# Performance work log

Hardware: AMD Instinct MI355X
Metric: run time of the kernel (lower is better)

The kernel has to match this reference:

```python
import jax, jax.numpy as jnp
import numpy as np

ALPHA = 0.1
MAX_ITER = 35
TOL = 0.01
STEP = ALPHA / 2.0  # step_size = alpha/2 as in TV2DFunction.forward


def _prox_tv1d(step, y):
    """Exact 1D TV prox via taut-string lower/upper hulls (faithful port of _prox_tv1d)."""
    n = y.shape[0]
    width = n + 1
    dt = y.dtype
    cs = jnp.cumsum(y)
    y_low = jnp.concatenate([jnp.zeros(1, dt), cs - step]).at[width - 1].add(step)
    y_up = jnp.concatenate([jnp.zeros(1, dt), cs + step]).at[width - 1].add(-step)

    inf = jnp.asarray(jnp.inf, dt)
    il = jnp.zeros(width, jnp.int32)   # index_low
    iu = jnp.zeros(width, jnp.int32)   # index_up
    idx = jnp.zeros(width, jnp.int32)  # breakpoint indices
    sl = jnp.zeros(width, dt).at[0].set(inf)    # slope_low
    su = jnp.zeros(width, dt).at[0].set(-inf)   # slope_up
    z = jnp.zeros(width, dt)
    zero = jnp.int32(0)

    def fdiv(num, a, b):
        # a > b always holds on the taken branch; maximum() only guards the
        # unselected jnp.where branch against NaN/Inf.
        return num / jnp.maximum(a - b, 1).astype(dt)

    def body(i, st):
        il, sl, iu, su, idx, z, s_l, c_l, s_u, c_u, c = st
        c_l = c_l + 1
        c_u = c_u + 1
        il = il.at[c_l].set(i)
        iu = iu.at[c_u].set(i)
        sl = sl.at[c_l].set(y_low[i] - y_low[i - 1])

        def w1_cond(t):
            il_, sl_, c_l_ = t
            return (c_l_ > s_l + 1) & (sl_[jnp.maximum(s_l, c_l_ - 1)] <= sl_[c_l_])

        def w1_body(t):
            il_, sl_, c_l_ = t
            c_l_ = c_l_ - 1
            il_ = il_.at[c_l_].set(i)
            ns = jnp.where(c_l_ > s_l + 1,
                           fdiv(y_low[i] - y_low[il_[c_l_ - 1]], i, il_[c_l_ - 1]),
                           fdiv(y_low[i] - z[c], i, idx[c]))
            return il_, sl_.at[c_l_].set(ns), c_l_

        il, sl, c_l = jax.lax.while_loop(w1_cond, w1_body, (il, sl, c_l))

        su = su.at[c_u].set(y_up[i] - y_up[i - 1])

        def w2_cond(t):
            iu_, su_, c_u_ = t
            return (c_u_ > s_u + 1) & (su_[jnp.maximum(s_u, c_u_ - 1)] >= su_[c_u_])

        def w2_body(t):
            iu_, su_, c_u_ = t
            c_u_ = c_u_ - 1
            iu_ = iu_.at[c_u_].set(i)
            ns = jnp.where(c_u_ > s_u + 1,
                           fdiv(y_up[i] - y_up[iu_[c_u_ - 1]], i, iu_[c_u_ - 1]),
                           fdiv(y_up[i] - z[c], i, idx[c]))
            return iu_, su_.at[c_u_].set(ns), c_u_

        iu, su, c_u = jax.lax.while_loop(w2_cond, w2_body, (iu, su, c_u))

        def w3_cond(t):
            idx_, z_, sl_, il_, s_u_, c_ = t
            return (c_l == s_l + 1) & (c_u > s_u_ + 1) & (sl_[c_l] >= su[s_u_ + 1])

        def w3_body(t):
            idx_, z_, sl_, il_, s_u_, c_ = t
            c_ = c_ + 1
            s_u_ = s_u_ + 1
            k = iu[s_u_]
            idx_ = idx_.at[c_].set(k)
            z_ = z_.at[c_].set(y_up[k])
            il_ = il_.at[s_l].set(k)
            sl_ = sl_.at[c_l].set(fdiv(y_low[i] - y_up[k], i, k))
            return idx_, z_, sl_, il_, s_u_, c_

        idx, z, sl, il, s_u, c = jax.lax.while_loop(w3_cond, w3_body, (idx, z, sl, il, s_u, c))

        def w4_cond(t):
            idx_, z_, su_, iu_, s_l_, c_ = t
            return (c_u == s_u + 1) & (c_l > s_l_ + 1) & (su_[c_u] <= sl[s_l_ + 1])

        def w4_body(t):
            idx_, z_, su_, iu_, s_l_, c_ = t
            c_ = c_ + 1
            s_l_ = s_l_ + 1
            k = il[s_l_]
            idx_ = idx_.at[c_].set(k)
            z_ = z_.at[c_].set(y_low[k])
            iu_ = iu_.at[s_u].set(k)
            su_ = su_.at[c_u].set(fdiv(y_up[i] - y_low[k], i, k))
            return idx_, z_, su_, iu_, s_l_, c_

        idx, z, su, iu, s_l, c = jax.lax.while_loop(w4_cond, w4_body, (idx, z, su, iu, s_l, c))

        return il, sl, iu, su, idx, z, s_l, c_l, s_u, c_u, c

    st = (il, sl, iu, su, idx, z, zero, zero, zero, zero, zero)
    il, sl, iu, su, idx, z, s_l, c_l, s_u, c_u, c = jax.lax.fori_loop(1, width, body, st)

    # tail: append remaining lower-hull points to the breakpoint list
    m = c_l - s_l
    offs = jnp.arange(width)
    valid = (offs >= 1) & (offs <= m)
    src = il[jnp.clip(s_l + offs, 0, width - 1)]
    tgt = jnp.where(valid, c + offs, width)  # 'width' is out of bounds -> dropped
    idx = idx.at[tgt].set(src, mode='drop')
    z = z.at[tgt].set(y_low[src], mode='drop')
    c = c + m

    # piecewise-constant output: slope of taut string on each segment
    a = (z - jnp.roll(z, 1)) / jnp.maximum(idx - jnp.roll(idx, 1), 1).astype(dt)
    knots = jnp.where(offs <= c, idx, n + 1)  # sorted; idx[c] == n
    seg = jnp.searchsorted(knots, jnp.arange(n), side='right')  # segment id in [1, c]
    return a[seg]


def _prox_cols(step, A):
    return jax.vmap(lambda col: _prox_tv1d(step, col), in_axes=1, out_axes=1)(A)


def _prox_rows(step, A):
    return jax.vmap(lambda row: _prox_tv1d(step, row))(A)


def _prox_tv2d(x, step, max_iter, tol):
    """Douglas-Rachford splitting for 2D TV prox (Barbero & Sra 2014)."""
    def cond(carry):
        it, x_, p, q, acc = carry
        return (it < max_iter) & (acc >= tol)

    def body(carry):
        it, x_, p, q, _ = carry
        y = _prox_cols(step, x_ + p)
        p = p + x_ - y
        x2 = _prox_rows(step, y + q)
        q = q + y - x2
        acc = jnp.max(jnp.abs(y - x2))
        return it + 1, x2, p, q, acc

    z0 = jnp.zeros_like(x)
    init = (jnp.int32(0), x, z0, z0, jnp.asarray(jnp.inf, x.dtype))
    return jax.lax.while_loop(cond, body, init)[1]


def setup_inputs() -> dict:
    key = jax.random.key(0)
    X = jax.random.normal(key, (256, 256), dtype=jnp.float32)
    return {"X": X}


def reference(X):
    return _prox_tv2d(X, STEP, MAX_ITER, TOL)
```

## Files before the change

kernel.cpp:

```cpp
#include <hip/hip_runtime.h>

#define N 256
#define NLINE 4
#define NB (N / NLINE)
#define NT (NLINE * 64)
#define LAM 0.05f
#define TWOLAM (2.0f * LAM)
#define FOURLAM (4.0f * LAM)
#define MAXIT 35
#define TOL 0.01f
#define SLOTSTRIDE 4

__device__ __forceinline__ float rlane(float v, int lane) {
    return __int_as_float(__builtin_amdgcn_readlane(__float_as_int(v), lane));
}

__device__ __forceinline__ void gstore(float* p, float v) {
    __hip_atomic_store(p, v, __ATOMIC_RELAXED, __HIP_MEMORY_SCOPE_AGENT);
}
__device__ __forceinline__ float4 gload4(const float* p) {
    float4 r;
    asm volatile("global_load_dwordx4 %0, %1, off sc0 sc1\n\ts_waitcnt vmcnt(0)"
                 : "=&v"(r) : "v"(p) : "memory");
    return r;
}

struct Dist { float r0, r1, r2, r3; };

__device__ __forceinline__ float dfetch(const Dist& d, int k) {
    const int lane = k & 63;
    const int sel = k >> 6;
    float a = rlane(d.r0, lane);
    float b = rlane(d.r1, lane);
    float c = rlane(d.r2, lane);
    float e = rlane(d.r3, lane);
    float ab = (sel & 1) ? b : a;
    float ce = (sel & 1) ? e : c;
    return (sel & 2) ? ce : ab;
}

__device__ __forceinline__ void flushseg(Dist& o, int lo, int hi, float val, int lane) {
    const unsigned len = (unsigned)(hi - lo);
    const int base = lane - lo;
    o.r0 = ((unsigned)(base      ) <= len) ? val : o.r0;
    o.r1 = ((unsigned)(base + 64 ) <= len) ? val : o.r1;
    o.r2 = ((unsigned)(base + 128) <= len) ? val : o.r2;
    o.r3 = ((unsigned)(base + 192) <= len) ? val : o.r3;
}

__device__ __forceinline__ unsigned long long sel4(unsigned long long a, unsigned long long b,
                                                   unsigned long long c, unsigned long long d, int r) {
    unsigned long long ab = (r & 1) ? b : a;
    unsigned long long cd = (r & 1) ? d : c;
    return (r & 2) ? cd : ab;
}

__device__ __forceinline__ unsigned wredmax(unsigned x) {
    unsigned t;
    t = (unsigned)__builtin_amdgcn_update_dpp(0, (int)x, 0x111, 0xf, 0xf, true); x = x > t ? x : t;
    t = (unsigned)__builtin_amdgcn_update_dpp(0, (int)x, 0x112, 0xf, 0xf, true); x = x > t ? x : t;
    t = (unsigned)__builtin_amdgcn_update_dpp(0, (int)x, 0x114, 0xf, 0xf, true); x = x > t ? x : t;
    t = (unsigned)__builtin_amdgcn_update_dpp(0, (int)x, 0x118, 0xf, 0xf, true); x = x > t ? x : t;
    t = (unsigned)__builtin_amdgcn_update_dpp(0, (int)x, 0x142, 0xf, 0xf, true); x = x > t ? x : t;
    t = (unsigned)__builtin_amdgcn_update_dpp(0, (int)x, 0x143, 0xf, 0xf, true); x = x > t ? x : t;
    return (unsigned)__builtin_amdgcn_readlane((int)x, 63);
}

__device__ void tv1d_scan(const Dist& v, Dist& o, const int lane)
{
    const float lam = LAM, mlam = -LAM, twolam = TWOLAM;

    Dist vnx;
    {
        float a0 = __shfl_down(v.r0, 1), a1 = __shfl_down(v.r1, 1);
        float a2 = __shfl_down(v.r2, 1), a3 = __shfl_down(v.r3, 1);
        const bool hi = (lane == 63);
        vnx.r0 = hi ? rlane(v.r1, 0) : a0;
        vnx.r1 = hi ? rlane(v.r2, 0) : a1;
        vnx.r2 = hi ? rlane(v.r3, 0) : a2;
        vnx.r3 = hi ? v.r3 : a3;
    }
    Dist d;
    d.r0 = vnx.r0 - v.r0;  d.r1 = vnx.r1 - v.r1;
    d.r2 = vnx.r2 - v.r2;  d.r3 = vnx.r3 - v.r3;
    const unsigned lambits = __float_as_uint(lam);
    Dist sl;
    sl.r0 = __uint_as_float((__float_as_uint(d.r0) & 0x80000000u) | lambits);
    sl.r1 = __uint_as_float((__float_as_uint(d.r1) & 0x80000000u) | lambits);
    sl.r2 = __uint_as_float((__float_as_uint(d.r2) & 0x80000000u) | lambits);
    sl.r3 = __uint_as_float((__float_as_uint(d.r3) & 0x80000000u) | lambits);
    Dist slp;
    {
        float b0 = __shfl_up(sl.r0, 1), b1 = __shfl_up(sl.r1, 1);
        float b2 = __shfl_up(sl.r2, 1), b3 = __shfl_up(sl.r3, 1);
        const bool lo = (lane == 0);
        slp.r0 = lo ? 0.0f : b0;
        slp.r1 = lo ? rlane(sl.r0, 63) : b1;
        slp.r2 = lo ? rlane(sl.r1, 63) : b2;
        slp.r3 = lo ? rlane(sl.r2, 63) : b3;
    }
    Dist e, g;
    {
        float t0 = v.r0 - slp.r0, t1 = v.r1 - slp.r1, t2 = v.r2 - slp.r2, t3 = v.r3 - slp.r3;
        e.r0 = t0 + sl.r0;  e.r1 = t1 + sl.r1;  e.r2 = t2 + sl.r2;  e.r3 = t3 + sl.r3;
        g.r0 = t0 - lam;    g.r1 = t1 - lam;    g.r2 = t2 - lam;    g.r3 = t3 - lam;
    }
    const unsigned long long S0 = __ballot(d.r0 < 0.0f);
    const unsigned long long S1 = __ballot(d.r1 < 0.0f);
    const unsigned long long S2 = __ballot(d.r2 < 0.0f);
    const unsigned long long S3 = __ballot(d.r3 < 0.0f);
    const unsigned long long B20 = __ballot(fabsf(d.r0) > TWOLAM);
    const unsigned long long B21 = __ballot(fabsf(d.r1) > TWOLAM);
    const unsigned long long B22 = __ballot(fabsf(d.r2) > TWOLAM);
    const unsigned long long B23 = __ballot(fabsf(d.r3) > TWOLAM);
    const unsigned long long B40 = __ballot(fabsf(d.r0) > FOURLAM);
    const unsigned long long B41 = __ballot(fabsf(d.r1) > FOURLAM);
    const unsigned long long B42 = __ballot(fabsf(d.r2) > FOURLAM);
    const unsigned long long B43 = __ballot(fabsf(d.r3) > FOURLAM);
    const unsigned long long Sp0 = (S0 << 1);
    const unsigned long long Sp1 = (S1 << 1) | (S0 >> 63);
    const unsigned long long Sp2 = (S2 << 1) | (S1 >> 63);
    const unsigned long long Sp3 = (S3 << 1) | (S2 >> 63);
    const unsigned long long NF0 = ~(B40 | (B20 & ~(S0 ^ Sp0)));
    const unsigned long long NF1 = ~(B41 | (B21 & ~(S1 ^ Sp1)));
    const unsigned long long NF2 = ~(B42 | (B22 & ~(S2 ^ Sp2)));
    const unsigned long long NF3 = ~((B43 | (B23 & ~(S3 ^ Sp3))) & 0x7FFFFFFFFFFFFFFFull);
    const unsigned long long FNn0 = (S0 & B20) | (~S0 & B40);
    const unsigned long long FNn1 = (S1 & B21) | (~S1 & B41);
    const unsigned long long FNn2 = (S2 & B22) | (~S2 & B42);
    const unsigned long long FNn3 = (S3 & B23) | (~S3 & B43);
    const unsigned long long FNp0 = (~S0 & B20) | (S0 & B40);
    const unsigned long long FNp1 = (~S1 & B21) | (S1 & B41);
    const unsigned long long FNp2 = (~S2 & B22) | (S2 & B42);
    const unsigned long long FNp3 = (~S3 & B23) | (S3 & B43);
    const int initFF = (int)(B40 & 1ull);

    auto firstnf = [&](int jmin) -> int {
        const int w = jmin >> 6;
        unsigned long long m = sel4(NF0, NF1, NF2, NF3, w) >> (jmin & 63);
        if (m) return jmin + (int)__builtin_ctzll(m);
        unsigned long long m1 = (w < 1) ? NF1 : 0ull;
        unsigned long long m2 = (w < 2) ? NF2 : 0ull;
        if (m1) return 64 + (int)__builtin_ctzll(m1);
        if (m2) return 128 + (int)__builtin_ctzll(m2);
        return 192 + (int)__builtin_ctzll(NF3);
    };

    auto trigbit = [&](int kk, int neg) -> int {
        const int w = kk >> 6;
        const unsigned long long m = neg ? sel4(FNn0, FNn1, FNn2, FNn3, w)
                                         : sel4(FNp0, FNp1, FNp2, FNp3, w);
        return (int)((m >> (kk & 63)) & 1ull);
    };

    int k = 0, k0 = 0, km = 0, kp = 0;
    float umin = lam, umax = mlam;
    const float v0 = rlane(v.r0, 0);
    float vmin = v0 - lam, vmax = v0 + lam;
    float flen = 1.0f;
    float rnext = 0.5f;
    float vn1 = rlane(vnx.r0, 0);

    auto fastfwd = [&]() {
        const int K1 = firstnf(k + 1);
        const int sneg = (int)((sel4(S0, S1, S2, S3, k >> 6) >> (k & 63)) & 1ull);
        flushseg(o, k, k, sneg ? vmin : vmax, lane);
        if (K1 > k + 1) {
            const int lo = k + 1;
            const unsigned len = (unsigned)(K1 - 1 - lo);
            const int base = lane - lo;
            o.r0 = ((unsigned)(base      ) <= len) ? e.r0 : o.r0;
            o.r1 = ((unsigned)(base + 64 ) <= len) ? e.r1 : o.r1;
            o.r2 = ((unsigned)(base + 128) <= len) ? e.r2 : o.r2;
            o.r3 = ((unsigned)(base + 192) <= len) ? e.r3 : o.r3;
        }
        k = K1; k0 = K1; km = K1; kp = K1;
        vmin = dfetch(g, K1);
        vmax = vmin + twolam;
        umin = lam; umax = mlam;
        flen = 1.0f; rnext = 0.5f;
        vn1 = dfetch(vnx, K1);
    };

    auto do_step = [&]() {
        const float pf_nj = dfetch(vnx, k + 1);
        const float pf_n  = dfetch(vnx, km + 1);
        const float pf_p  = dfetch(vnx, kp + 1);
        const float un = umin + vn1 - vmin;
        const float ux = umax + vn1 - vmax;
        const bool neg = un < mlam;
        const bool pos = ux > lam;
        const int wn = (k + 1) >> 6, bn = (k + 1) & 63;
        const int tn = (int)((sel4(FNn0, FNn1, FNn2, FNn3, wn) >> bn) & 1ull);
        const int tp = (int)((sel4(FNp0, FNp1, FNp2, FNp3, wn) >> bn) & 1ull);
        if (__builtin_expect((int)(neg | pos), 1)) {
            const float fval = neg ? vmin : vmax;
            const int   fhi  = neg ? km : kp;
            flushseg(o, k0, fhi, fval, lane);
            const int k0n = fhi + 1;
            float vstar;
            int trig;
            if (__builtin_expect((int)(k0n <= k), 0)) {
                vstar = dfetch(v, k0n);
                trig = trigbit(k0n, (int)neg);
            } else {
                vstar = vn1;
                trig = neg ? tn : tp;
            }
            k = k0n; k0 = k0n; km = k0n; kp = k0n;
            vmin = neg ? vstar : vstar - twolam;
            vmax = vmin + twolam;
            umin = lam; umax = mlam;
            flen = 1.0f; rnext = 0.5f;
            if (k < N - 1 && trig) {
                fastfwd();
            } else {
                vn1 = neg ? pf_n : pf_p;
            }
        } else {
            k++;
            const float r = rnext;
            flen += 1.0f;
            const bool cmin = (un >= lam);
            const bool cmax = (ux <= mlam);
            vmin = cmin ? fmaf(un - lam, r, vmin) : vmin;
            km   = cmin ? k : km;
            umin = cmin ? lam : un;
            vmax = cmax ? fmaf(ux + lam, r, vmax) : vmax;
            kp   = cmax ? k : kp;
            umax = cmax ? mlam : ux;
            vn1 = pf_nj;
            rnext = __builtin_amdgcn_rcpf(flen + 1.0f);
        }
    };

    if (initFF) fastfwd();

    for (;;) {
        while (k < N - 1) {
            do_step();
            if (k >= N - 1) break;
            do_step();
        }
        for (;;) {
            if (umin < 0.0f) {
                flushseg(o, k0, km, vmin, lane);
                k0 = km + 1;
                if (k0 > N - 1) return;
                km = k = k0;
                vmin = dfetch(v, k0);
                umin = lam;
                umax = vmin + lam - vmax;
                flen = 1.0f;
            } else if (umax > 0.0f) {
                flushseg(o, k0, kp, vmax, lane);
                k0 = kp + 1;
                if (k0 > N - 1) return;
                kp = k = k0;
                vmax = dfetch(v, k0);
                umax = mlam;
                umin = vmax - lam - vmin;
                flen = 1.0f;
            } else {
                vmin += umin / flen;
                flushseg(o, k0, k, vmin, lane);
                return;
            }
            if (k != N - 1) break;
        }
        rnext = 0.5f;
        vn1 = dfetch(vnx, k);
    }
}

template <bool WANT>
__device__ __forceinline__ unsigned wavebar(unsigned long long* slots, unsigned seq,
                                            unsigned payload, int line, int lane, int wave,
                                            unsigned long long* s_rel)
{
    __builtin_amdgcn_s_waitcnt(0);
    __hip_atomic_store(&slots[line * SLOTSTRIDE],
                       ((unsigned long long)payload << 32) | (unsigned long long)seq,
                       __ATOMIC_RELAXED, __HIP_MEMORY_SCOPE_AGENT);
    unsigned ga = 0u;
    if (wave == 0) {
        auto ld = [&](int i) {
            return __hip_atomic_load(&slots[i * SLOTSTRIDE],
                                     __ATOMIC_RELAXED, __HIP_MEMORY_SCOPE_AGENT);
        };
        unsigned long long f0 = ld(lane), f1 = ld(lane + 64),
                           f2 = ld(lane + 128), f3 = ld(lane + 192);
        for (;;) {
            unsigned long long g0 = ld(lane), g1 = ld(lane + 64),
                               g2 = ld(lane + 128), g3 = ld(lane + 192);
            const bool ok = ((unsigned)f0 >= seq) & ((unsigned)f1 >= seq) &
                            ((unsigned)f2 >= seq) & ((unsigned)f3 >= seq);
            if (__all((int)ok)) break;
            f0 = g0; f1 = g1; f2 = g2; f3 = g3;
        }
        if (WANT) {
            unsigned a = (unsigned)(f0 >> 32), b = (unsigned)(f1 >> 32);
            unsigned c = (unsigned)(f2 >> 32), d = (unsigned)(f3 >> 32);
            a = a > b ? a : b;  c = c > d ? c : d;  a = a > c ? a : c;
            ga = wredmax(a);
        }
        if (lane == 0)
            __hip_atomic_store(s_rel, ((unsigned long long)ga << 32) | (unsigned long long)seq,
                               __ATOMIC_RELAXED, __HIP_MEMORY_SCOPE_WORKGROUP);
    } else {
        unsigned long long r;
        do {
            r = __hip_atomic_load(s_rel, __ATOMIC_RELAXED, __HIP_MEMORY_SCOPE_WORKGROUP);
        } while ((unsigned)r < seq);
        if (WANT) ga = (unsigned)(r >> 32);
    }
    return ga;
}

__global__ __launch_bounds__(NT) void tv2d_coop(const float* __restrict__ X,
                                                float* __restrict__ xw,
                                                float* __restrict__ y,
                                                unsigned long long* __restrict__ slots)
{
    const int t = threadIdx.x;
    const int lane = t & 63;
    const int wave = t >> 6;
    const int line = blockIdx.x * NLINE + wave;
    const int col4 = 4 * blockIdx.x;
    __shared__ float tile[N * 5];
    __shared__ unsigned long long s_rel;
    if (t == 0) s_rel = 0ull;

    Dist p = {0.f, 0.f, 0.f, 0.f};
    Dist q = {0.f, 0.f, 0.f, 0.f};
    unsigned accprev = 0u;

    for (int it = 0; it < MAXIT; ++it) {
        const float* xs = (it == 0) ? X : xw;
        const float4 xc = gload4(xs + t * N + col4);
        tile[t * 5 + 0] = xc.x;
        tile[t * 5 + 1] = xc.y;
        tile[t * 5 + 2] = xc.z;
        tile[t * 5 + 3] = xc.w;
        __syncthreads();
        Dist v, o;
        v.r0 = tile[(lane      ) * 5 + wave] + p.r0;
        v.r1 = tile[(lane + 64 ) * 5 + wave] + p.r1;
        v.r2 = tile[(lane + 128) * 5 + wave] + p.r2;
        v.r3 = tile[(lane + 192) * 5 + wave] + p.r3;
        tv1d_scan(v, o, lane);
        p.r0 = v.r0 - o.r0;  p.r1 = v.r1 - o.r1;
        p.r2 = v.r2 - o.r2;  p.r3 = v.r3 - o.r3;
        float* yt = y + line * N;
        gstore(yt + lane,       o.r0);
        gstore(yt + lane + 64,  o.r1);
        gstore(yt + lane + 128, o.r2);
        gstore(yt + lane + 192, o.r3);
        wavebar<false>(slots, 2u * (unsigned)it + 1u, accprev, line, lane, wave, &s_rel);

        const float4 yc = gload4(y + t * N + col4);
        tile[t * 5 + 0] = yc.x;
        tile[t * 5 + 1] = yc.y;
        tile[t * 5 + 2] = yc.z;
        tile[t * 5 + 3] = yc.w;
        __syncthreads();
        float y0 = tile[(lane      ) * 5 + wave];
        float y1 = tile[(lane + 64 ) * 5 + wave];
        float y2 = tile[(lane + 128) * 5 + wave];
        float y3 = tile[(lane + 192) * 5 + wave];
        Dist w, o2;
        w.r0 = y0 + q.r0;
        w.r1 = y1 + q.r1;
        w.r2 = y2 + q.r2;
        w.r3 = y3 + q.r3;
        tv1d_scan(w, o2, lane);
        float d0 = y0 - o2.r0;
        float d1 = y1 - o2.r1;
        float d2 = y2 - o2.r2;
        float d3 = y3 - o2.r3;
        q.r0 = w.r0 - o2.r0;  q.r1 = w.r1 - o2.r1;
        q.r2 = w.r2 - o2.r2;  q.r3 = w.r3 - o2.r3;
        float* xr = xw + line * N;
        gstore(xr + lane,       o2.r0);
        gstore(xr + lane + 64,  o2.r1);
        gstore(xr + lane + 128, o2.r2);
        gstore(xr + lane + 192, o2.r3);

        float am = fmaxf(fmaxf(fabsf(d0), fabsf(d1)), fmaxf(fabsf(d2), fabsf(d3)));
        const unsigned acc = wredmax(__float_as_uint(am));

        if (it == MAXIT - 1) break;

        const unsigned ga = wavebar<true>(slots, 2u * (unsigned)it + 2u, acc, line, lane, wave, &s_rel);
        if (__uint_as_float(ga) < TOL) break;
        accprev = acc;
    }
}

extern "C" void kernel_launch(void* const* d_in, const int* in_sizes, int n_in,
                              void* d_out, int out_size, void* d_ws, size_t ws_size,
                              hipStream_t stream) {
    const float* X = (const float*)d_in[0];
    float* xw = (float*)d_out;
    float* y = (float*)d_ws;
    unsigned long long* slots = (unsigned long long*)((char*)d_ws + (size_t)N * N * sizeof(float));
    (void)hipMemsetAsync((void*)slots, 0, N * SLOTSTRIDE * sizeof(unsigned long long), stream);
    void* args[] = { (void*)&X, (void*)&xw, (void*)&y, (void*)&slots };
    (void)hipLaunchCooperativeKernel((void*)tv2d_coop, dim3(NB), dim3(NT), args, 0, stream);
}
```

Before: 310.9 us.

## Use one wave per block and drop LDS tile transpose and in-block barrier

```diff
diff --git a/kernel.cpp b/kernel.cpp
--- a/kernel.cpp
+++ b/kernel.cpp
@@ -1,15 +1,14 @@
 #include <hip/hip_runtime.h>
 
 #define N 256
-#define NLINE 4
-#define NB (N / NLINE)
-#define NT (NLINE * 64)
+#define NB 256
+#define NT 64
 #define LAM 0.05f
 #define TWOLAM (2.0f * LAM)
 #define FOURLAM (4.0f * LAM)
 #define MAXIT 35
 #define TOL 0.01f
-#define SLOTSTRIDE 4
+#define SLOTSTRIDE 2
 
 __device__ __forceinline__ float rlane(float v, int lane) {
     return __int_as_float(__builtin_amdgcn_readlane(__float_as_int(v), lane));
@@ -18,11 +17,21 @@
 __device__ __forceinline__ void gstore(float* p, float v) {
     __hip_atomic_store(p, v, __ATOMIC_RELAXED, __HIP_MEMORY_SCOPE_AGENT);
 }
-__device__ __forceinline__ float4 gload4(const float* p) {
-    float4 r;
-    asm volatile("global_load_dwordx4 %0, %1, off sc0 sc1\n\ts_waitcnt vmcnt(0)"
-                 : "=&v"(r) : "v"(p) : "memory");
-    return r;
+
+__device__ __forceinline__ void gload_col(const float* mat, int c, int lane, float& a,
+                                          float& b, float& d, float& e) {
+    const float* p0 = mat + (size_t)lane * N + c;
+    const float* p1 = p0 + 64 * N;
+    const float* p2 = p0 + 128 * N;
+    const float* p3 = p0 + 192 * N;
+    asm volatile("global_load_dword %0, %4, off sc0 sc1\n\t"
+                 "global_load_dword %1, %5, off sc0 sc1\n\t"
+                 "global_load_dword %2, %6, off sc0 sc1\n\t"
+                 "global_load_dword %3, %7, off sc0 sc1\n\t"
+                 "s_waitcnt vmcnt(0)"
+                 : "=&v"(a), "=&v"(b), "=&v"(d), "=&v"(e)
+                 : "v"(p0), "v"(p1), "v"(p2), "v"(p3)
+                 : "memory");
 }
 
 struct Dist { float r0, r1, r2, r3; };
@@ -183,9 +192,6 @@
     };
 
     auto do_step = [&]() {
-        const float pf_nj = dfetch(vnx, k + 1);
-        const float pf_n  = dfetch(vnx, km + 1);
-        const float pf_p  = dfetch(vnx, kp + 1);
         const float un = umin + vn1 - vmin;
         const float ux = umax + vn1 - vmax;
         const bool neg = un < mlam;
@@ -215,7 +221,7 @@
             if (k < N - 1 && trig) {
                 fastfwd();
             } else {
-                vn1 = neg ? pf_n : pf_p;
+                vn1 = dfetch(vnx, k);
             }
         } else {
             k++;
@@ -229,7 +235,7 @@
             vmax = cmax ? fmaf(ux + lam, r, vmax) : vmax;
             kp   = cmax ? k : kp;
             umax = cmax ? mlam : ux;
-            vn1 = pf_nj;
+            vn1 = dfetch(vnx, k);
             rnext = __builtin_amdgcn_rcpf(flen + 1.0f);
         }
     };
@@ -275,61 +281,43 @@
 
 template <bool WANT>
 __device__ __forceinline__ unsigned wavebar(unsigned long long* slots, unsigned seq,
-                                            unsigned payload, int line, int lane, int wave,
-                                            unsigned long long* s_rel)
+                                            unsigned payload, int line, int lane)
 {
     __builtin_amdgcn_s_waitcnt(0);
     __hip_atomic_store(&slots[line * SLOTSTRIDE],
                        ((unsigned long long)payload << 32) | (unsigned long long)seq,
                        __ATOMIC_RELAXED, __HIP_MEMORY_SCOPE_AGENT);
+    auto ld = [&](int i) {
+        return __hip_atomic_load(&slots[i * SLOTSTRIDE],
+                                 __ATOMIC_RELAXED, __HIP_MEMORY_SCOPE_AGENT);
+    };
+    unsigned long long f0 = ld(lane), f1 = ld(lane + 64),
+                       f2 = ld(lane + 128), f3 = ld(lane + 192);
+    for (;;) {
+        unsigned long long g0 = ld(lane), g1 = ld(lane + 64),
+                           g2 = ld(lane + 128), g3 = ld(lane + 192);
+        const bool ok = ((unsigned)f0 >= seq) & ((unsigned)f1 >= seq) &
+                        ((unsigned)f2 >= seq) & ((unsigned)f3 >= seq);
+        if (__all((int)ok)) break;
+        f0 = g0; f1 = g1; f2 = g2; f3 = g3;
+    }
     unsigned ga = 0u;
-    if (wave == 0) {
-        auto ld = [&](int i) {
-            return __hip_atomic_load(&slots[i * SLOTSTRIDE],
-                                     __ATOMIC_RELAXED, __HIP_MEMORY_SCOPE_AGENT);
-        };
-        unsigned long long f0 = ld(lane), f1 = ld(lane + 64),
-                           f2 = ld(lane + 128), f3 = ld(lane + 192);
-        for (;;) {
-            unsigned long long g0 = ld(lane), g1 = ld(lane + 64),
-                               g2 = ld(lane + 128), g3 = ld(lane + 192);
-            const bool ok = ((unsigned)f0 >= seq) & ((unsigned)f1 >= seq) &
-                            ((unsigned)f2 >= seq) & ((unsigned)f3 >= seq);
-            if (__all((int)ok)) break;
-            f0 = g0; f1 = g1; f2 = g2; f3 = g3;
-        }
-        if (WANT) {
-            unsigned a = (unsigned)(f0 >> 32), b = (unsigned)(f1 >> 32);
-            unsigned c = (unsigned)(f2 >> 32), d = (unsigned)(f3 >> 32);
-            a = a > b ? a : b;  c = c > d ? c : d;  a = a > c ? a : c;
-            ga = wredmax(a);
-        }
-        if (lane == 0)
-            __hip_atomic_store(s_rel, ((unsigned long long)ga << 32) | (unsigned long long)seq,
-                               __ATOMIC_RELAXED, __HIP_MEMORY_SCOPE_WORKGROUP);
-    } else {
-        unsigned long long r;
-        do {
-            r = __hip_atomic_load(s_rel, __ATOMIC_RELAXED, __HIP_MEMORY_SCOPE_WORKGROUP);
-        } while ((unsigned)r < seq);
-        if (WANT) ga = (unsigned)(r >> 32);
+    if (WANT) {
+        unsigned a = (unsigned)(f0 >> 32), b = (unsigned)(f1 >> 32);
+        unsigned c = (unsigned)(f2 >> 32), d = (unsigned)(f3 >> 32);
+        a = a > b ? a : b;  c = c > d ? c : d;  a = a > c ? a : c;
+        ga = wredmax(a);
     }
     return ga;
 }
 
 __global__ __launch_bounds__(NT) void tv2d_coop(const float* __restrict__ X,
                                                 float* __restrict__ xw,
-                                                float* __restrict__ y,
+                                                float* __restrict__ yt,
                                                 unsigned long long* __restrict__ slots)
 {
-    const int t = threadIdx.x;
-    const int lane = t & 63;
-    const int wave = t >> 6;
-    const int line = blockIdx.x * NLINE + wave;
-    const int col4 = 4 * blockIdx.x;
-    __shared__ float tile[N * 5];
-    __shared__ unsigned long long s_rel;
-    if (t == 0) s_rel = 0ull;
+    const int lane = threadIdx.x;
+    const int b = blockIdx.x;
 
     Dist p = {0.f, 0.f, 0.f, 0.f};
     Dist q = {0.f, 0.f, 0.f, 0.f};
@@ -337,63 +325,46 @@
 
     for (int it = 0; it < MAXIT; ++it) {
         const float* xs = (it == 0) ? X : xw;
-        const float4 xc = gload4(xs + t * N + col4);
-        tile[t * 5 + 0] = xc.x;
-        tile[t * 5 + 1] = xc.y;
-        tile[t * 5 + 2] = xc.z;
-        tile[t * 5 + 3] = xc.w;
-        __syncthreads();
         Dist v, o;
-        v.r0 = tile[(lane      ) * 5 + wave] + p.r0;
-        v.r1 = tile[(lane + 64 ) * 5 + wave] + p.r1;
-        v.r2 = tile[(lane + 128) * 5 + wave] + p.r2;
-        v.r3 = tile[(lane + 192) * 5 + wave] + p.r3;
+        gload_col(xs, b, lane, v.r0, v.r1, v.r2, v.r3);
+        v.r0 += p.r0;  v.r1 += p.r1;  v.r2 += p.r2;  v.r3 += p.r3;
         tv1d_scan(v, o, lane);
         p.r0 = v.r0 - o.r0;  p.r1 = v.r1 - o.r1;
         p.r2 = v.r2 - o.r2;  p.r3 = v.r3 - o.r3;
-        float* yt = y + line * N;
-        gstore(yt + lane,       o.r0);
-        gstore(yt + lane + 64,  o.r1);
-        gstore(yt + lane + 128, o.r2);
-        gstore(yt + lane + 192, o.r3);
-        wavebar<false>(slots, 2u * (unsigned)it + 1u, accprev, line, lane, wave, &s_rel);
-
-        const float4 yc = gload4(y + t * N + col4);
-        tile[t * 5 + 0] = yc.x;
-        tile[t * 5 + 1] = yc.y;
-        tile[t * 5 + 2] = yc.z;
-        tile[t * 5 + 3] = yc.w;
-        __syncthreads();
-        float y0 = tile[(lane      ) * 5 + wave];
-        float y1 = tile[(lane + 64 ) * 5 + wave];
-        float y2 = tile[(lane + 128) * 5 + wave];
-        float y3 = tile[(lane + 192) * 5 + wave];
-        Dist w, o2;
-        w.r0 = y0 + q.r0;
-        w.r1 = y1 + q.r1;
-        w.r2 = y2 + q.r2;
-        w.r3 = y3 + q.r3;
+        float* yr = yt + b * N;
+        gstore(yr + lane,       o.r0);
+        gstore(yr + lane + 64,  o.r1);
+        gstore(yr + lane + 128, o.r2);
+        gstore(yr + lane + 192, o.r3);
+        wavebar<false>(slots, 2u * (unsigned)it + 1u, accprev, b, lane);
+
+        Dist yv, w, o2;
+        gload_col(yt, b, lane, yv.r0, yv.r1, yv.r2, yv.r3);
+        w.r0 = yv.r0 + q.r0;
+        w.r1 = yv.r1 + q.r1;
+        w.r2 = yv.r2 + q.r2;
+        w.r3 = yv.r3 + q.r3;
         tv1d_scan(w, o2, lane);
-        float d0 = y0 - o2.r0;
-        float d1 = y1 - o2.r1;
-        float d2 = y2 - o2.r2;
-        float d3 = y3 - o2.r3;
+        float d0 = yv.r0 - o2.r0;
+        float d1 = yv.r1 - o2.r1;
+        float d2 = yv.r2 - o2.r2;
+        float d3 = yv.r3 - o2.r3;
         q.r0 = w.r0 - o2.r0;  q.r1 = w.r1 - o2.r1;
         q.r2 = w.r2 - o2.r2;  q.r3 = w.r3 - o2.r3;
-        float* xr = xw + line * N;
+        float* xr = xw + b * N;
         gstore(xr + lane,       o2.r0);
         gstore(xr + lane + 64,  o2.r1);
         gstore(xr + lane + 128, o2.r2);
         gstore(xr + lane + 192, o2.r3);
 
         float am = fmaxf(fmaxf(fabsf(d0), fabsf(d1)), fmaxf(fabsf(d2), fabsf(d3)));
-        const unsigned acc = wredmax(__float_as_uint(am));
+        const unsigned amu = wredmax(__float_as_uint(am));
 
         if (it == MAXIT - 1) break;
 
-        const unsigned ga = wavebar<true>(slots, 2u * (unsigned)it + 2u, acc, line, lane, wave, &s_rel);
+        const unsigned ga = wavebar<true>(slots, 2u * (unsigned)it + 2u, amu, b, lane);
         if (__uint_as_float(ga) < TOL) break;
-        accprev = acc;
+        accprev = amu;
     }
 }
 
@@ -402,9 +373,9 @@
                               hipStream_t stream) {
     const float* X = (const float*)d_in[0];
     float* xw = (float*)d_out;
-    float* y = (float*)d_ws;
+    float* yt = (float*)d_ws;
     unsigned long long* slots = (unsigned long long*)((char*)d_ws + (size_t)N * N * sizeof(float));
     (void)hipMemsetAsync((void*)slots, 0, N * SLOTSTRIDE * sizeof(unsigned long long), stream);
-    void* args[] = { (void*)&X, (void*)&xw, (void*)&y, (void*)&slots };
+    void* args[] = { (void*)&X, (void*)&xw, (void*)&yt, (void*)&slots };
     (void)hipLaunchCooperativeKernel((void*)tv2d_coop, dim3(NB), dim3(NT), args, 0, stream);
 }
```

After: 271.1 us. -12.8%, faster.
